# Performance work log

Measured on AMD Instinct MI355X. Metric: run time of the kernel, lower is better.

The kernel has to match this reference:

```python
import jax, jax.numpy as jnp
import numpy as np

N = 100000
E = 1600000
G = 2048          # number of graphs in the batch
F_IN = 22
H = 64
OUT = 1
EPS = 1e-5


def setup_inputs() -> dict:
    key = jax.random.key(0)
    ks = jax.random.split(key, 12)
    x = jax.random.normal(ks[0], (N, F_IN), dtype=jnp.float32)
    edge_index = jax.random.randint(ks[1], (2, E), 0, N, dtype=jnp.int32)
    batch = jnp.sort(jax.random.randint(ks[2], (N,), 0, G, dtype=jnp.int32))
    def lin(k, fan_out, fan_in):
        s = 1.0 / np.sqrt(fan_in)
        return jax.random.uniform(k, (fan_out, fan_in), jnp.float32, -s, s)
    return {
        "x": x, "edge_index": edge_index, "batch": batch,
        "W1": lin(ks[3], H, F_IN), "b1": jnp.zeros((H,), jnp.float32),
        "g1": jnp.ones((H,), jnp.float32), "be1": jnp.zeros((H,), jnp.float32),
        "W2": lin(ks[4], H, H), "b2": jnp.zeros((H,), jnp.float32),
        "g2": jnp.ones((H,), jnp.float32), "be2": jnp.zeros((H,), jnp.float32),
        "fcw1": lin(ks[5], H // 2, H), "fcb1": jnp.zeros((H // 2,), jnp.float32),
        "fcw2": lin(ks[6], OUT, H // 2), "fcb2": jnp.zeros((OUT,), jnp.float32),
    }


def _gcn_conv(x, src, dst, W, b):
    # PyG GCNConv: linear transform, add self-loops, symmetric D^-1/2 A D^-1/2 aggregation, + bias
    h = x @ W.T                                   # [N, out]
    loops = jnp.arange(N, dtype=src.dtype)
    s = jnp.concatenate([src, loops])             # [E+N]
    d = jnp.concatenate([dst, loops])
    deg = jax.ops.segment_sum(jnp.ones_like(d, dtype=h.dtype), d, num_segments=N)
    dinv = jax.lax.rsqrt(deg)                     # deg >= 1 due to self-loops
    norm = dinv[s] * dinv[d]                      # [E+N]
    msg = h[s] * norm[:, None]                    # [E+N, out] gather
    out = jax.ops.segment_sum(msg, d, num_segments=N)  # scatter-add
    return out + b


def _batchnorm(x, g, be):
    mu = jnp.mean(x, axis=0)
    var = jnp.mean((x - mu) ** 2, axis=0)
    return g * (x - mu) * jax.lax.rsqrt(var + EPS) + be


def reference(x, edge_index, batch, W1, b1, g1, be1, W2, b2, g2, be2,
              fcw1, fcb1, fcw2, fcb2):
    src, dst = edge_index[0], edge_index[1]
    h = _gcn_conv(x, src, dst, W1, b1)
    h = jax.nn.relu(_batchnorm(h, g1, be1))       # dropout = identity (eval)
    h = _gcn_conv(h, src, dst, W2, b2)
    h = jax.nn.relu(_batchnorm(h, g2, be2))
    # global mean pool over graphs
    sums = jax.ops.segment_sum(h, batch, num_segments=G)            # [G, H]
    cnts = jax.ops.segment_sum(jnp.ones((N,), h.dtype), batch, num_segments=G)
    pooled = sums / jnp.maximum(cnts, 1.0)[:, None]
    z = jax.nn.relu(pooled @ fcw1.T + fcb1)
    return z @ fcw2.T + fcb2                      # [G, OUT]
```

## Files before the change

kernel.cpp:

```cpp
#include <hip/hip_runtime.h>

static constexpr int Nn  = 100000;
static constexpr int Ne  = 1600000;
static constexpr int Gg  = 2048;
static constexpr int Fin = 22;
static constexpr float EPSf = 1e-5f;
static constexpr int NBLK = (Nn + 255) / 256;

__global__ void k_init(int* cnt, double* stats) {
    int i = blockIdx.x * blockDim.x + threadIdx.x;
    int stride = gridDim.x * blockDim.x;
    for (int j = i; j < Nn; j += stride) cnt[j] = 0;
    for (int j = i; j < 256; j += stride) stats[j] = 0.0;
}

__global__ void k_pad(const float* __restrict__ x, float* __restrict__ xp) {
    int idx = blockIdx.x * blockDim.x + threadIdx.x;
    if (idx >= Nn * 6) return;
    int n = idx / 6, q = idx - n * 6;
    float4 v;
    int f0 = q * 4;
    const float* xr = x + n * Fin;
    v.x = (f0 + 0 < Fin) ? xr[f0 + 0] : 0.f;
    v.y = (f0 + 1 < Fin) ? xr[f0 + 1] : 0.f;
    v.z = (f0 + 2 < Fin) ? xr[f0 + 2] : 0.f;
    v.w = (f0 + 3 < Fin) ? xr[f0 + 3] : 0.f;
    ((float4*)xp)[idx] = v;
}

__global__ void k_count(const int* __restrict__ dst, int* cnt) {
    int e = blockIdx.x * blockDim.x + threadIdx.x;
    if (e < Ne) atomicAdd(&cnt[dst[e]], 1);
}

__global__ __launch_bounds__(256) void k_scan1(const int* __restrict__ cnt,
                                               int* row_ptr, int* bsum) {
    __shared__ int sh[256];
    int t = threadIdx.x, b = blockIdx.x;
    int i = b * 256 + t;
    int v = (i < Nn) ? cnt[i] : 0;
    sh[t] = v;
    __syncthreads();
    for (int off = 1; off < 256; off <<= 1) {
        int a = (t >= off) ? sh[t - off] : 0;
        __syncthreads();
        sh[t] += a;
        __syncthreads();
    }
    if (i < Nn) row_ptr[i] = sh[t] - v;
    if (t == 255) bsum[b] = sh[255];
}

__global__ __launch_bounds__(512) void k_scan2(int* bsum) {
    __shared__ int sh[512];
    int t = threadIdx.x;
    int v = (t < NBLK) ? bsum[t] : 0;
    sh[t] = v;
    __syncthreads();
    for (int off = 1; off < 512; off <<= 1) {
        int a = (t >= off) ? sh[t - off] : 0;
        __syncthreads();
        sh[t] += a;
        __syncthreads();
    }
    if (t < NBLK) bsum[t] = sh[t] - v;
}

__global__ __launch_bounds__(256) void k_scan3(const int* __restrict__ cnt,
                                               const int* __restrict__ bsum,
                                               int* row_ptr, int* cursor, float* dinv) {
    int i = blockIdx.x * blockDim.x + threadIdx.x;
    if (i >= Nn) return;
    int r = row_ptr[i] + bsum[i >> 8];
    row_ptr[i] = r;
    cursor[i] = r;
    dinv[i] = rsqrtf(1.0f + (float)cnt[i]);
    if (i == 0) row_ptr[Nn] = Ne;
}

__global__ void k_fill(const int* __restrict__ src, const int* __restrict__ dst,
                       const float* __restrict__ dinv, int* cursor, int2* csr) {
    int e = blockIdx.x * blockDim.x + threadIdx.x;
    if (e >= Ne) return;
    int s = src[e], d = dst[e];
    int pos = atomicAdd(&cursor[d], 1);
    csr[pos] = make_int2(s, __float_as_int(dinv[s] * dinv[d]));
}

__global__ __launch_bounds__(256) void k_gather1(const int* __restrict__ row_ptr,
                                                 const int2* __restrict__ csr,
                                                 const float* __restrict__ dinv,
                                                 const float* __restrict__ xp,
                                                 float* __restrict__ outp) {
    int idx = blockIdx.x * blockDim.x + threadIdx.x;
    if (idx >= Nn * 6) return;
    int n = idx / 6, q = idx - n * 6;
    const float4* h4 = (const float4*)xp;
    float di = dinv[n];
    float sl = di * di;
    float4 hv = h4[n * 6 + q];
    float4 acc;
    acc.x = hv.x * sl; acc.y = hv.y * sl; acc.z = hv.z * sl; acc.w = hv.w * sl;
    int e = row_ptr[n], e1 = row_ptr[n + 1];
    for (; e + 1 < e1; e += 2) {
        int2 ea = csr[e], eb = csr[e + 1];
        float na = __int_as_float(ea.y), nb = __int_as_float(eb.y);
        float4 va = h4[ea.x * 6 + q];
        float4 vb = h4[eb.x * 6 + q];
        acc.x += va.x * na + vb.x * nb;
        acc.y += va.y * na + vb.y * nb;
        acc.z += va.z * na + vb.z * nb;
        acc.w += va.w * na + vb.w * nb;
    }
    if (e < e1) {
        int2 ea = csr[e];
        float na = __int_as_float(ea.y);
        float4 va = h4[ea.x * 6 + q];
        acc.x += va.x * na; acc.y += va.y * na; acc.z += va.z * na; acc.w += va.w * na;
    }
    ((float4*)outp)[n * 6 + q] = acc;
}

__global__ __launch_bounds__(256) void k_gemm1(const float* __restrict__ aggx,
                                               const float* __restrict__ W1,
                                               const float* __restrict__ b1,
                                               float* __restrict__ out) {
    __shared__ float Wl[64 * 23];
    __shared__ float Xl[4][24];
    int tid = threadIdx.x;
    for (int i = tid; i < 64 * Fin; i += 256) {
        int o = i / Fin, k = i % Fin;
        Wl[o * 23 + k] = W1[i];
    }
    int f = tid & 63, ln = tid >> 6;
    float bf = b1[f];
    for (int base = blockIdx.x * 4; base < Nn; base += gridDim.x * 4) {
        __syncthreads();
        if (tid < 24) {
            int r = tid / 6, q = tid - (tid / 6) * 6;
            if (base + r < Nn)
                *((float4*)&Xl[r][q * 4]) = ((const float4*)aggx)[(base + r) * 6 + q];
        }
        __syncthreads();
        int n = base + ln;
        if (n < Nn) {
            float s = bf;
            #pragma unroll
            for (int k = 0; k < Fin; k++) s += Xl[ln][k] * Wl[f * 23 + k];
            out[n * 64 + f] = s;
        }
    }
}

__global__ __launch_bounds__(256) void k_bnstats(const float* __restrict__ a, double* stats) {
    __shared__ float ssum[256], ssq[256];
    int tid = threadIdx.x;
    int f = tid & 63, ln = tid >> 6;
    float s = 0.f, q = 0.f;
    for (int n = blockIdx.x * 4 + ln; n < Nn; n += gridDim.x * 4) {
        float v = a[n * 64 + f];
        s += v;
        q += v * v;
    }
    ssum[tid] = s; ssq[tid] = q;
    __syncthreads();
    if (tid < 64) {
        s = ssum[tid] + ssum[tid + 64] + ssum[tid + 128] + ssum[tid + 192];
        q = ssq[tid] + ssq[tid + 64] + ssq[tid + 128] + ssq[tid + 192];
        atomicAdd(&stats[f], (double)s);
        atomicAdd(&stats[64 + f], (double)q);
    }
}

__global__ __launch_bounds__(256) void k_gemm2(const float* __restrict__ xin,
                                               const float* __restrict__ W2,
                                               const double* __restrict__ stats,
                                               const float* __restrict__ g,
                                               const float* __restrict__ be,
                                               float* __restrict__ out) {
    __shared__ float Wl[64 * 65];
    __shared__ float Xl[4][64];
    int tid = threadIdx.x;
    for (int i = tid; i < 64 * 64; i += 256) {
        int o = i >> 6, k = i & 63;
        Wl[o * 65 + k] = W2[i];
    }
    int f = tid & 63, ln = tid >> 6;
    double mu = stats[f] / (double)Nn;
    double var = stats[64 + f] / (double)Nn - mu * mu;
    float sc = rsqrtf((float)var + EPSf) * g[f];
    float muf = (float)mu;
    float bef = be[f];
    for (int base = blockIdx.x * 4; base < Nn; base += gridDim.x * 4) {
        __syncthreads();
        int n = base + ln;
        if (n < Nn) {
            float v = (xin[n * 64 + f] - muf) * sc + bef;
            Xl[ln][f] = v > 0.f ? v : 0.f;
        }
        __syncthreads();
        if (n < Nn) {
            float s = 0.f;
            #pragma unroll
            for (int k = 0; k < 64; k++) s += Xl[ln][k] * Wl[f * 65 + k];
            out[n * 64 + f] = s;
        }
    }
}

__global__ __launch_bounds__(256) void k_gather2(const int* __restrict__ row_ptr,
                                                 const int2* __restrict__ csr,
                                                 const float* __restrict__ dinv,
                                                 const float* __restrict__ h,
                                                 const float* __restrict__ bias,
                                                 float* __restrict__ out) {
    int idx = blockIdx.x * blockDim.x + threadIdx.x;
    if (idx >= Nn * 16) return;
    int n = idx >> 4, q = idx & 15;
    const float4* h4 = (const float4*)h;
    float di = dinv[n];
    float sl = di * di;
    float4 acc = ((const float4*)bias)[q];
    float4 hv = h4[n * 16 + q];
    acc.x += hv.x * sl; acc.y += hv.y * sl; acc.z += hv.z * sl; acc.w += hv.w * sl;
    int e = row_ptr[n], e1 = row_ptr[n + 1];
    for (; e + 1 < e1; e += 2) {
        int2 ea = csr[e], eb = csr[e + 1];
        float na = __int_as_float(ea.y), nb = __int_as_float(eb.y);
        float4 va = h4[ea.x * 16 + q];
        float4 vb = h4[eb.x * 16 + q];
        acc.x += va.x * na + vb.x * nb;
        acc.y += va.y * na + vb.y * nb;
        acc.z += va.z * na + vb.z * nb;
        acc.w += va.w * na + vb.w * nb;
    }
    if (e < e1) {
        int2 ea = csr[e];
        float na = __int_as_float(ea.y);
        float4 va = h4[ea.x * 16 + q];
        acc.x += va.x * na; acc.y += va.y * na; acc.z += va.z * na; acc.w += va.w * na;
    }
    ((float4*)out)[n * 16 + q] = acc;
}

__global__ __launch_bounds__(64) void k_poolmlp(const float* __restrict__ a,
                                                const int* __restrict__ batch,
                                                const double* __restrict__ stats,
                                                const float* __restrict__ g,
                                                const float* __restrict__ be,
                                                const float* __restrict__ fcw1,
                                                const float* __restrict__ fcb1,
                                                const float* __restrict__ fcw2,
                                                const float* __restrict__ fcb2,
                                                float* __restrict__ out) {
    __shared__ float p[64];
    int gidx = blockIdx.x;
    int tid = threadIdx.x;
    int lo = 0, hi = Nn;
    while (lo < hi) { int m = (lo + hi) >> 1; if (batch[m] < gidx) lo = m + 1; else hi = m; }
    int start = lo;
    hi = Nn;
    while (lo < hi) { int m = (lo + hi) >> 1; if (batch[m] < gidx + 1) lo = m + 1; else hi = m; }
    int end = lo;
    double mu = stats[tid] / (double)Nn;
    double var = stats[64 + tid] / (double)Nn - mu * mu;
    float sc = rsqrtf((float)var + EPSf) * g[tid];
    float muf = (float)mu;
    float bef = be[tid];
    float s = 0.f;
    for (int n = start; n < end; n++) {
        float v = (a[n * 64 + tid] - muf) * sc + bef;
        s += v > 0.f ? v : 0.f;
    }
    int cnt = end - start;
    float c = cnt < 1 ? 1.f : (float)cnt;
    p[tid] = s / c;
    __syncthreads();
    float w = 0.f;
    if (tid < 32) {
        float z = fcb1[tid];
        #pragma unroll
        for (int k = 0; k < 64; k++) z += p[k] * fcw1[tid * 64 + k];
        z = z > 0.f ? z : 0.f;
        w = z * fcw2[tid];
    }
    for (int off = 16; off; off >>= 1) w += __shfl_down(w, off);
    if (tid == 0) out[gidx] = w + fcb2[0];
}

extern "C" void kernel_launch(void* const* d_in, const int* in_sizes, int n_in,
                              void* d_out, int out_size, void* d_ws, size_t ws_size,
                              hipStream_t stream) {
    const float* x    = (const float*)d_in[0];
    const int* ei     = (const int*)d_in[1];
    const int* src    = ei;
    const int* dst    = ei + Ne;
    const int* batch  = (const int*)d_in[2];
    const float* W1   = (const float*)d_in[3];
    const float* b1   = (const float*)d_in[4];
    const float* g1   = (const float*)d_in[5];
    const float* be1  = (const float*)d_in[6];
    const float* W2   = (const float*)d_in[7];
    const float* b2   = (const float*)d_in[8];
    const float* g2   = (const float*)d_in[9];
    const float* be2  = (const float*)d_in[10];
    const float* fcw1 = (const float*)d_in[11];
    const float* fcb1 = (const float*)d_in[12];
    const float* fcw2 = (const float*)d_in[13];
    const float* fcb2 = (const float*)d_in[14];
    float* out = (float*)d_out;

    double* stats1  = (double*)d_ws;
    double* stats2  = stats1 + 128;
    int2*   csr     = (int2*)(stats2 + 128);
    float*  bufA    = (float*)(csr + Ne);
    float*  bufB    = bufA + Nn * 64;
    float*  dinv    = bufB + Nn * 64;
    int*    cnt     = (int*)(dinv + Nn);
    int*    row_ptr = cnt + Nn;
    int*    cursor  = row_ptr + Nn + 1;
    int*    bsum    = cursor + Nn;

    k_init<<<512, 256, 0, stream>>>(cnt, stats1);
    k_pad<<<(Nn * 6 + 255) / 256, 256, 0, stream>>>(x, bufA);
    k_count<<<(Ne + 255) / 256, 256, 0, stream>>>(dst, cnt);
    k_scan1<<<NBLK, 256, 0, stream>>>(cnt, row_ptr, bsum);
    k_scan2<<<1, 512, 0, stream>>>(bsum);
    k_scan3<<<NBLK, 256, 0, stream>>>(cnt, bsum, row_ptr, cursor, dinv);
    k_fill<<<(Ne + 255) / 256, 256, 0, stream>>>(src, dst, dinv, cursor, csr);

    k_gather1<<<(Nn * 6 + 255) / 256, 256, 0, stream>>>(row_ptr, csr, dinv, bufA, bufB);
    k_gemm1<<<1024, 256, 0, stream>>>(bufB, W1, b1, bufA);
    k_bnstats<<<512, 256, 0, stream>>>(bufA, stats1);

    k_gemm2<<<2048, 256, 0, stream>>>(bufA, W2, stats1, g1, be1, bufB);
    k_gather2<<<(Nn * 16 + 255) / 256, 256, 0, stream>>>(row_ptr, csr, dinv, bufB, b2, bufA);
    k_bnstats<<<512, 256, 0, stream>>>(bufA, stats2);

    k_poolmlp<<<Gg, 64, 0, stream>>>(bufA, batch, stats2, g2, be2,
                                     fcw1, fcb1, fcw2, fcb2, out);
}
```

Measured before the change: 486.4 us.

## Factor symmetric GCN normalization into pre/post dinv scaling, drop per-edge weights

Rewrites D^-1/2 A D^-1/2 aggregation by pre-scaling node features by dinv (in k_pad and the gemm2 epilogue) and post-scaling the gathered sum by dinv, so the CSR stores only source indices instead of (src, norm) pairs. This halves CSR edge traffic in fill and both gathers and removes the dinv[s] random read in k_fill. The gather loops are also unrolled by four with independent accumulators for more memory-level parallelism. Summation order changes, which may shift floating-point results slightly.

```diff
diff --git a/kernel.cpp b/kernel.cpp
--- a/kernel.cpp
+++ b/kernel.cpp
@@ -12,20 +12,6 @@
     int stride = gridDim.x * blockDim.x;
     for (int j = i; j < Nn; j += stride) cnt[j] = 0;
     for (int j = i; j < 256; j += stride) stats[j] = 0.0;
-}
-
-__global__ void k_pad(const float* __restrict__ x, float* __restrict__ xp) {
-    int idx = blockIdx.x * blockDim.x + threadIdx.x;
-    if (idx >= Nn * 6) return;
-    int n = idx / 6, q = idx - n * 6;
-    float4 v;
-    int f0 = q * 4;
-    const float* xr = x + n * Fin;
-    v.x = (f0 + 0 < Fin) ? xr[f0 + 0] : 0.f;
-    v.y = (f0 + 1 < Fin) ? xr[f0 + 1] : 0.f;
-    v.z = (f0 + 2 < Fin) ? xr[f0 + 2] : 0.f;
-    v.w = (f0 + 3 < Fin) ? xr[f0 + 3] : 0.f;
-    ((float4*)xp)[idx] = v;
 }
 
 __global__ void k_count(const int* __restrict__ dst, int* cnt) {
@@ -78,17 +64,32 @@
     if (i == 0) row_ptr[Nn] = Ne;
 }
 
+__global__ void k_pad(const float* __restrict__ x, const float* __restrict__ dinv,
+                      float* __restrict__ xp) {
+    int idx = blockIdx.x * blockDim.x + threadIdx.x;
+    if (idx >= Nn * 6) return;
+    int n = idx / 6, q = idx - n * 6;
+    float di = dinv[n];
+    float4 v;
+    int f0 = q * 4;
+    const float* xr = x + n * Fin;
+    v.x = (f0 + 0 < Fin) ? xr[f0 + 0] * di : 0.f;
+    v.y = (f0 + 1 < Fin) ? xr[f0 + 1] * di : 0.f;
+    v.z = (f0 + 2 < Fin) ? xr[f0 + 2] * di : 0.f;
+    v.w = (f0 + 3 < Fin) ? xr[f0 + 3] * di : 0.f;
+    ((float4*)xp)[idx] = v;
+}
+
 __global__ void k_fill(const int* __restrict__ src, const int* __restrict__ dst,
-                       const float* __restrict__ dinv, int* cursor, int2* csr) {
+                       int* cursor, int* __restrict__ csr_src) {
     int e = blockIdx.x * blockDim.x + threadIdx.x;
     if (e >= Ne) return;
-    int s = src[e], d = dst[e];
-    int pos = atomicAdd(&cursor[d], 1);
-    csr[pos] = make_int2(s, __float_as_int(dinv[s] * dinv[d]));
+    int pos = atomicAdd(&cursor[dst[e]], 1);
+    csr_src[pos] = src[e];
 }
 
 __global__ __launch_bounds__(256) void k_gather1(const int* __restrict__ row_ptr,
-                                                 const int2* __restrict__ csr,
+                                                 const int* __restrict__ csr_src,
                                                  const float* __restrict__ dinv,
                                                  const float* __restrict__ xp,
                                                  float* __restrict__ outp) {
@@ -97,28 +98,33 @@
     int n = idx / 6, q = idx - n * 6;
     const float4* h4 = (const float4*)xp;
     float di = dinv[n];
-    float sl = di * di;
-    float4 hv = h4[n * 6 + q];
-    float4 acc;
-    acc.x = hv.x * sl; acc.y = hv.y * sl; acc.z = hv.z * sl; acc.w = hv.w * sl;
+    float4 a0 = h4[n * 6 + q];
+    float4 a1 = make_float4(0.f, 0.f, 0.f, 0.f);
+    float4 a2 = make_float4(0.f, 0.f, 0.f, 0.f);
+    float4 a3 = make_float4(0.f, 0.f, 0.f, 0.f);
     int e = row_ptr[n], e1 = row_ptr[n + 1];
-    for (; e + 1 < e1; e += 2) {
-        int2 ea = csr[e], eb = csr[e + 1];
-        float na = __int_as_float(ea.y), nb = __int_as_float(eb.y);
-        float4 va = h4[ea.x * 6 + q];
-        float4 vb = h4[eb.x * 6 + q];
-        acc.x += va.x * na + vb.x * nb;
-        acc.y += va.y * na + vb.y * nb;
-        acc.z += va.z * na + vb.z * nb;
-        acc.w += va.w * na + vb.w * nb;
-    }
-    if (e < e1) {
-        int2 ea = csr[e];
-        float na = __int_as_float(ea.y);
-        float4 va = h4[ea.x * 6 + q];
-        acc.x += va.x * na; acc.y += va.y * na; acc.z += va.z * na; acc.w += va.w * na;
-    }
-    ((float4*)outp)[n * 6 + q] = acc;
+    for (; e + 3 < e1; e += 4) {
+        int s0 = csr_src[e], s1 = csr_src[e + 1], s2 = csr_src[e + 2], s3 = csr_src[e + 3];
+        float4 v0 = h4[s0 * 6 + q];
+        float4 v1 = h4[s1 * 6 + q];
+        float4 v2 = h4[s2 * 6 + q];
+        float4 v3 = h4[s3 * 6 + q];
+        a0.x += v0.x; a0.y += v0.y; a0.z += v0.z; a0.w += v0.w;
+        a1.x += v1.x; a1.y += v1.y; a1.z += v1.z; a1.w += v1.w;
+        a2.x += v2.x; a2.y += v2.y; a2.z += v2.z; a2.w += v2.w;
+        a3.x += v3.x; a3.y += v3.y; a3.z += v3.z; a3.w += v3.w;
+    }
+    for (; e < e1; e++) {
+        int s = csr_src[e];
+        float4 v = h4[s * 6 + q];
+        a0.x += v.x; a0.y += v.y; a0.z += v.z; a0.w += v.w;
+    }
+    float4 r;
+    r.x = (a0.x + a1.x + a2.x + a3.x) * di;
+    r.y = (a0.y + a1.y + a2.y + a3.y) * di;
+    r.z = (a0.z + a1.z + a2.z + a3.z) * di;
+    r.w = (a0.w + a1.w + a2.w + a3.w) * di;
+    ((float4*)outp)[n * 6 + q] = r;
 }
 
 __global__ __launch_bounds__(256) void k_gemm1(const float* __restrict__ aggx,
@@ -177,6 +183,7 @@
                                                const double* __restrict__ stats,
                                                const float* __restrict__ g,
                                                const float* __restrict__ be,
+                                               const float* __restrict__ dinv,
                                                float* __restrict__ out) {
     __shared__ float Wl[64 * 65];
     __shared__ float Xl[4][64];
@@ -203,13 +210,13 @@
             float s = 0.f;
             #pragma unroll
             for (int k = 0; k < 64; k++) s += Xl[ln][k] * Wl[f * 65 + k];
-            out[n * 64 + f] = s;
+            out[n * 64 + f] = s * dinv[n];
         }
     }
 }
 
 __global__ __launch_bounds__(256) void k_gather2(const int* __restrict__ row_ptr,
-                                                 const int2* __restrict__ csr,
+                                                 const int* __restrict__ csr_src,
                                                  const float* __restrict__ dinv,
                                                  const float* __restrict__ h,
                                                  const float* __restrict__ bias,
@@ -219,28 +226,34 @@
     int n = idx >> 4, q = idx & 15;
     const float4* h4 = (const float4*)h;
     float di = dinv[n];
-    float sl = di * di;
-    float4 acc = ((const float4*)bias)[q];
-    float4 hv = h4[n * 16 + q];
-    acc.x += hv.x * sl; acc.y += hv.y * sl; acc.z += hv.z * sl; acc.w += hv.w * sl;
+    float4 bv = ((const float4*)bias)[q];
+    float4 a0 = h4[n * 16 + q];
+    float4 a1 = make_float4(0.f, 0.f, 0.f, 0.f);
+    float4 a2 = make_float4(0.f, 0.f, 0.f, 0.f);
+    float4 a3 = make_float4(0.f, 0.f, 0.f, 0.f);
     int e = row_ptr[n], e1 = row_ptr[n + 1];
-    for (; e + 1 < e1; e += 2) {
-        int2 ea = csr[e], eb = csr[e + 1];
-        float na = __int_as_float(ea.y), nb = __int_as_float(eb.y);
-        float4 va = h4[ea.x * 16 + q];
-        float4 vb = h4[eb.x * 16 + q];
-        acc.x += va.x * na + vb.x * nb;
-        acc.y += va.y * na + vb.y * nb;
-        acc.z += va.z * na + vb.z * nb;
-        acc.w += va.w * na + vb.w * nb;
-    }
-    if (e < e1) {
-        int2 ea = csr[e];
-        float na = __int_as_float(ea.y);
-        float4 va = h4[ea.x * 16 + q];
-        acc.x += va.x * na; acc.y += va.y * na; acc.z += va.z * na; acc.w += va.w * na;
-    }
-    ((float4*)out)[n * 16 + q] = acc;
+    for (; e + 3 < e1; e += 4) {
+        int s0 = csr_src[e], s1 = csr_src[e + 1], s2 = csr_src[e + 2], s3 = csr_src[e + 3];
+        float4 v0 = h4[s0 * 16 + q];
+        float4 v1 = h4[s1 * 16 + q];
+        float4 v2 = h4[s2 * 16 + q];
+        float4 v3 = h4[s3 * 16 + q];
+        a0.x += v0.x; a0.y += v0.y; a0.z += v0.z; a0.w += v0.w;
+        a1.x += v1.x; a1.y += v1.y; a1.z += v1.z; a1.w += v1.w;
+        a2.x += v2.x; a2.y += v2.y; a2.z += v2.z; a2.w += v2.w;
+        a3.x += v3.x; a3.y += v3.y; a3.z += v3.z; a3.w += v3.w;
+    }
+    for (; e < e1; e++) {
+        int s = csr_src[e];
+        float4 v = h4[s * 16 + q];
+        a0.x += v.x; a0.y += v.y; a0.z += v.z; a0.w += v.w;
+    }
+    float4 r;
+    r.x = (a0.x + a1.x + a2.x + a3.x) * di + bv.x;
+    r.y = (a0.y + a1.y + a2.y + a3.y) * di + bv.y;
+    r.z = (a0.z + a1.z + a2.z + a3.z) * di + bv.z;
+    r.w = (a0.w + a1.w + a2.w + a3.w) * di + bv.w;
+    ((float4*)out)[n * 16 + q] = r;
 }
 
 __global__ __launch_bounds__(64) void k_poolmlp(const float* __restrict__ a,
@@ -312,8 +325,8 @@
 
     double* stats1  = (double*)d_ws;
     double* stats2  = stats1 + 128;
-    int2*   csr     = (int2*)(stats2 + 128);
-    float*  bufA    = (float*)(csr + Ne);
+    int*    csr_src = (int*)(stats2 + 128);
+    float*  bufA    = (float*)(csr_src + Ne);
     float*  bufB    = bufA + Nn * 64;
     float*  dinv    = bufB + Nn * 64;
     int*    cnt     = (int*)(dinv + Nn);
@@ -322,19 +335,20 @@
     int*    bsum    = cursor + Nn;
 
     k_init<<<512, 256, 0, stream>>>(cnt, stats1);
-    k_pad<<<(Nn * 6 + 255) / 256, 256, 0, stream>>>(x, bufA);
     k_count<<<(Ne + 255) / 256, 256, 0, stream>>>(dst, cnt);
     k_scan1<<<NBLK, 256, 0, stream>>>(cnt, row_ptr, bsum);
     k_scan2<<<1, 512, 0, stream>>>(bsum);
     k_scan3<<<NBLK, 256, 0, stream>>>(cnt, bsum, row_ptr, cursor, dinv);
-    k_fill<<<(Ne + 255) / 256, 256, 0, stream>>>(src, dst, dinv, cursor, csr);
-
-    k_gather1<<<(Nn * 6 + 255) / 256, 256, 0, stream>>>(row_ptr, csr, dinv, bufA, bufB);
+
+    k_pad<<<(Nn * 6 + 255) / 256, 256, 0, stream>>>(x, dinv, bufA);
+    k_fill<<<(Ne + 255) / 256, 256, 0, stream>>>(src, dst, cursor, csr_src);
+
+    k_gather1<<<(Nn * 6 + 255) / 256, 256, 0, stream>>>(row_ptr, csr_src, dinv, bufA, bufB);
     k_gemm1<<<1024, 256, 0, stream>>>(bufB, W1, b1, bufA);
     k_bnstats<<<512, 256, 0, stream>>>(bufA, stats1);
 
-    k_gemm2<<<2048, 256, 0, stream>>>(bufA, W2, stats1, g1, be1, bufB);
-    k_gather2<<<(Nn * 16 + 255) / 256, 256, 0, stream>>>(row_ptr, csr, dinv, bufB, b2, bufA);
+    k_gemm2<<<2048, 256, 0, stream>>>(bufA, W2, stats1, g1, be1, dinv, bufB);
+    k_gather2<<<(Nn * 16 + 255) / 256, 256, 0, stream>>>(row_ptr, csr_src, dinv, bufB, b2, bufA);
     k_bnstats<<<512, 256, 0, stream>>>(bufA, stats2);
 
     k_poolmlp<<<Gg, 64, 0, stream>>>(bufA, batch, stats2, g2, be2,
```

After: 524.5 us. 1.08x slower.
